# Kernel optimization log

Hardware: AMD Instinct MI355X
Metric: run time of the kernel (lower is better)

The kernel has to match this reference:

```python
import jax, jax.numpy as jnp
import numpy as np

RATIO = 0.1

def setup_inputs() -> dict:
    key = jax.random.key(0)
    x = jax.random.normal(key, (8, 1024, 4096), dtype=jnp.float32)
    return {"x": x}

def reference(x):
    shape = x.shape
    xf = x.reshape(-1)                       # [N]
    k = int(RATIO * xf.shape[0])             # static k
    src, index = jax.lax.top_k(xf, k)         # values (not abs), matching torch.topk
    out = jnp.zeros_like(xf).at[index].set(src)
    return out.reshape(shape)
```

## Files before the change

kernel.cpp:

```cpp
#include <hip/hip_runtime.h>
#include <stdint.h>


#define BLK       256
#define MAXGRID   1024
#define NB1       4096
#define NBC       1024
#define STAGE_CAP 3072
#define EQ_CAP    65536
#define GRP_SHIFT 6
#define LSTRIDE   64

typedef float vf4 __attribute__((ext_vector_type(4)));

__device__ __forceinline__ unsigned f2u(float x) {
    unsigned b = __float_as_uint(x);
    return (b & 0x80000000u) ? ~b : (b | 0x80000000u);
}
__device__ __forceinline__ float u2f(unsigned u) {
    return __uint_as_float((u & 0x80000000u) ? (u & 0x7FFFFFFFu) : ~u);
}
__device__ __forceinline__ unsigned cload(const unsigned* p) {
    return __hip_atomic_load(p, __ATOMIC_RELAXED, __HIP_MEMORY_SCOPE_AGENT);
}
__device__ __forceinline__ void cstore(unsigned* p, unsigned v) {
    __hip_atomic_store(p, v, __ATOMIC_RELAXED, __HIP_MEMORY_SCOPE_AGENT);
}

__device__ __forceinline__ void gsync(unsigned* bw, unsigned ep, unsigned nbk) {
    __syncthreads();
    if (threadIdx.x == 0) {
        const unsigned g  = (unsigned)blockIdx.x >> GRP_SHIFT;
        const unsigned ng = (nbk + ((1u << GRP_SHIFT) - 1u)) >> GRP_SHIFT;
        unsigned* arr = bw;
        unsigned* gar = bw + 1024;
        unsigned* rel = bw + 1088;
        unsigned grp0 = g << GRP_SHIFT;
        unsigned cnt_g = nbk - grp0;
        if (cnt_g > (1u << GRP_SHIFT)) cnt_g = (1u << GRP_SHIFT);
        unsigned old = __hip_atomic_fetch_add(&arr[g * LSTRIDE], 1u,
                                              __ATOMIC_RELAXED, __HIP_MEMORY_SCOPE_AGENT);
        if (old == ep * cnt_g - 1u) {
            unsigned og = __hip_atomic_fetch_add(gar, 1u,
                                                 __ATOMIC_RELAXED, __HIP_MEMORY_SCOPE_AGENT);
            if (og == ep * ng - 1u) {
                for (unsigned i = 0; i < ng; ++i)
                    cstore(&rel[i * LSTRIDE], ep);
            }
        }
        unsigned spins = 0u;
        while (cload(&rel[g * LSTRIDE]) < ep) {
            __builtin_amdgcn_s_sleep(16);
            if (++spins > 1500000u) break;
        }
    }
    __syncthreads();
}

__device__ __forceinline__ unsigned block_exscan256(unsigned v,
                                                    volatile unsigned* lds,
                                                    int tid)
{
    lds[tid] = v;
    __syncthreads();
    for (int off = 1; off < 256; off <<= 1) {
        unsigned t = (tid >= off) ? lds[tid - off] : 0u;
        __syncthreads();
        lds[tid] += t;
        __syncthreads();
    }
    unsigned incl = lds[tid];
    return incl - v;
}

template<int NB, int PT>
__device__ void scan_desc(const unsigned* h, unsigned kin,
                          volatile unsigned* slds, unsigned* sb, int tid)
{
    unsigned loc[PT], partial = 0u;
#pragma unroll
    for (int i = 0; i < PT; ++i) {
        loc[i] = cload(&h[NB - 1 - (tid * PT + i)]);
        partial += loc[i];
    }
    unsigned cum = block_exscan256(partial, slds, tid);
#pragma unroll
    for (int i = 0; i < PT; ++i) {
        unsigned c = loc[i];
        if (cum < kin && cum + c >= kin) {
            sb[0] = (unsigned)(NB - 1 - (tid * PT + i));
            sb[1] = kin - cum;
            sb[2] = c;
        }
        cum += c;
    }
    __syncthreads();
}

__global__ void __launch_bounds__(BLK, 4)
topk_fused(const float* __restrict__ x, float* __restrict__ out,
           long long N, int n4, unsigned k,
           unsigned* __restrict__ sc, unsigned* __restrict__ bw,
           unsigned* __restrict__ hist_a, unsigned* __restrict__ hist_b,
           unsigned* __restrict__ hist_c, unsigned* __restrict__ hist_b2,
           unsigned* __restrict__ hist_c2, unsigned* __restrict__ eq_list)
{
    __shared__ unsigned lh[2 * NB1];
    __shared__ unsigned slds[BLK];
    __shared__ unsigned sb[8];

    const int tid = threadIdx.x;
    const int bid = blockIdx.x;
    const unsigned nbk = gridDim.x;
    const int stride = (int)nbk * BLK;
    unsigned ep = 0;

    const float4* x4 = (const float4*)x;
    const long long t0 = (long long)n4 * 4;
    const int ntail = (int)(N - t0);

    for (int i = tid; i < 2 * NB1; i += BLK) lh[i] = 0u;
    __syncthreads();
    {
        unsigned* my = lh + ((tid >> 7) & 1) * NB1;
        for (int i = bid * BLK + tid; i < n4; i += stride) {
            float4 v = x4[i];
            atomicAdd(&my[f2u(v.x) >> 20], 1u);
            atomicAdd(&my[f2u(v.y) >> 20], 1u);
            atomicAdd(&my[f2u(v.z) >> 20], 1u);
            atomicAdd(&my[f2u(v.w) >> 20], 1u);
        }
        if (bid == 0 && tid < ntail) atomicAdd(&my[f2u(x[t0 + tid]) >> 20], 1u);
    }
    __syncthreads();
    for (int i = tid; i < NB1; i += BLK) {
        unsigned s = lh[i] + lh[NB1 + i];
        if (s) atomicAdd(&hist_a[i], s);
    }
    gsync(bw, ++ep, nbk);

    scan_desc<NB1, 16>(hist_a, k, slds, sb, tid);
    const unsigned b1 = sb[0], krem = sb[1];
    __syncthreads();

    if (tid == 0) sb[3] = 0u;
    __syncthreads();
    unsigned* su = lh;
    unsigned* si = lh + STAGE_CAP;
    auto stage = [&](unsigned u, unsigned idxv) {
        unsigned p = atomicAdd(&sb[3], 1u);
        if (p < STAGE_CAP) { su[p] = u; si[p] = idxv; }
        else cstore(&sc[7], 1u);
    };
    for (int i = bid * BLK + tid; i < n4; i += stride) {
        float4 v = x4[i];
        unsigned u0 = f2u(v.x), u1 = f2u(v.y), u2 = f2u(v.z), u3 = f2u(v.w);
        bool c0 = (u0 >> 20) == b1, c1 = (u1 >> 20) == b1,
             c2 = (u2 >> 20) == b1, c3 = (u3 >> 20) == b1;
        vf4 o;
        o.x = ((u0 >> 20) > b1) ? v.x : 0.0f;
        o.y = ((u1 >> 20) > b1) ? v.y : 0.0f;
        o.z = ((u2 >> 20) > b1) ? v.z : 0.0f;
        o.w = ((u3 >> 20) > b1) ? v.w : 0.0f;
        if (!(c0 | c1 | c2 | c3)) {
            __builtin_nontemporal_store(o, (vf4*)out + i);
        } else {
            unsigned base = (unsigned)i * 4u;
            if (c0) stage(u0, base + 0u); else out[base + 0u] = o.x;
            if (c1) stage(u1, base + 1u); else out[base + 1u] = o.y;
            if (c2) stage(u2, base + 2u); else out[base + 2u] = o.z;
            if (c3) stage(u3, base + 3u); else out[base + 3u] = o.w;
        }
    }
    if (bid == 0 && tid < ntail) {
        long long idx = t0 + tid;
        float v = x[idx];
        unsigned u = f2u(v);
        if ((u >> 20) == b1) stage(u, (unsigned)idx);
        else out[idx] = ((u >> 20) > b1) ? v : 0.0f;
    }
    __syncthreads();
    const unsigned mycnt0 = sb[3];
    const unsigned mycnt = (mycnt0 > STAGE_CAP) ? STAGE_CAP : mycnt0;
    unsigned* chist = lh + 2 * STAGE_CAP;
    unsigned* chm = chist + ((tid >> 7) & 1) * NBC;
    for (int i = tid; i < 2 * NBC; i += BLK) chist[i] = 0u;
    __syncthreads();
    for (unsigned j = (unsigned)tid; j < mycnt; j += BLK)
        atomicAdd(&chm[(su[j] >> 10) & 1023u], 1u);
    __syncthreads();
    for (int i = tid; i < NBC; i += BLK) {
        unsigned s = chist[i] + chist[NBC + i];
        if (s) atomicAdd(&hist_b[i], s);
    }
    gsync(bw, ++ep, nbk);

    const bool ovf = (cload(&sc[7]) != 0u);

    if (!ovf) {
        scan_desc<NBC, 4>(hist_b, krem, slds, sb, tid);
        const unsigned b2 = sb[0], krem2 = sb[1];
        __syncthreads();

        for (int i = tid; i < 2 * NBC; i += BLK) chist[i] = 0u;
        __syncthreads();
        for (unsigned j = (unsigned)tid; j < mycnt; j += BLK) {
            unsigned u = su[j];
            if (((u >> 10) & 1023u) == b2) atomicAdd(&chm[u & 1023u], 1u);
        }
        __syncthreads();
        for (int i = tid; i < NBC; i += BLK) {
            unsigned s = chist[i] + chist[NBC + i];
            if (s) atomicAdd(&hist_c[i], s);
        }
        gsync(bw, ++ep, nbk);

        scan_desc<NBC, 4>(hist_c, krem2, slds, sb, tid);
        const unsigned b3 = sb[0], needeq = sb[1], ceq = sb[2];
        const unsigned tu = (b1 << 20) | (b2 << 10) | b3;
        const bool allties = (needeq == ceq);

        for (unsigned j = (unsigned)tid; j < mycnt; j += BLK) {
            unsigned u = su[j], idxv = si[j];
            if (u > tu)      out[idxv] = u2f(u);
            else if (u < tu) out[idxv] = 0.0f;
            else if (allties) out[idxv] = u2f(u);
            else { unsigned q = atomicAdd(&sc[5], 1u); if (q < EQ_CAP) cstore(&eq_list[q], idxv); }
        }
        if (!allties) {
            gsync(bw, ++ep, nbk);
            if (bid == 0) {
                unsigned m = cload(&sc[5]); if (m > EQ_CAP) m = EQ_CAP;
                float f = u2f(tu);
                for (unsigned j = (unsigned)tid; j < m; j += BLK) {
                    unsigned idxv = cload(&eq_list[j]);
                    unsigned cnt = 0u;
                    for (unsigned l = 0; l < m; ++l)
                        cnt += (cload(&eq_list[l]) < idxv) ? 1u : 0u;
                    out[idxv] = (cnt < needeq) ? f : 0.0f;
                }
            }
        }
    } else {
        for (int i = tid; i < 2 * NBC; i += BLK) chist[i] = 0u;
        __syncthreads();
        for (int i = bid * BLK + tid; i < n4; i += stride) {
            float4 v = x4[i];
            unsigned u;
            u = f2u(v.x); if ((u >> 20) == b1) atomicAdd(&chm[(u >> 10) & 1023u], 1u);
            u = f2u(v.y); if ((u >> 20) == b1) atomicAdd(&chm[(u >> 10) & 1023u], 1u);
            u = f2u(v.z); if ((u >> 20) == b1) atomicAdd(&chm[(u >> 10) & 1023u], 1u);
            u = f2u(v.w); if ((u >> 20) == b1) atomicAdd(&chm[(u >> 10) & 1023u], 1u);
        }
        if (bid == 0 && tid < ntail) {
            unsigned u = f2u(x[t0 + tid]);
            if ((u >> 20) == b1) atomicAdd(&chm[(u >> 10) & 1023u], 1u);
        }
        __syncthreads();
        for (int i = tid; i < NBC; i += BLK) {
            unsigned s = chist[i] + chist[NBC + i];
            if (s) atomicAdd(&hist_b2[i], s);
        }
        gsync(bw, ++ep, nbk);
        scan_desc<NBC, 4>(hist_b2, krem, slds, sb, tid);
        const unsigned b2 = sb[0], krem2 = sb[1];
        __syncthreads();

        for (int i = tid; i < 2 * NBC; i += BLK) chist[i] = 0u;
        __syncthreads();
        for (int i = bid * BLK + tid; i < n4; i += stride) {
            float4 v = x4[i];
            unsigned u;
            u = f2u(v.x); if ((u >> 20) == b1 && ((u >> 10) & 1023u) == b2) atomicAdd(&chm[u & 1023u], 1u);
            u = f2u(v.y); if ((u >> 20) == b1 && ((u >> 10) & 1023u) == b2) atomicAdd(&chm[u & 1023u], 1u);
            u = f2u(v.z); if ((u >> 20) == b1 && ((u >> 10) & 1023u) == b2) atomicAdd(&chm[u & 1023u], 1u);
            u = f2u(v.w); if ((u >> 20) == b1 && ((u >> 10) & 1023u) == b2) atomicAdd(&chm[u & 1023u], 1u);
        }
        if (bid == 0 && tid < ntail) {
            unsigned u = f2u(x[t0 + tid]);
            if ((u >> 20) == b1 && ((u >> 10) & 1023u) == b2) atomicAdd(&chm[u & 1023u], 1u);
        }
        __syncthreads();
        for (int i = tid; i < NBC; i += BLK) {
            unsigned s = chist[i] + chist[NBC + i];
            if (s) atomicAdd(&hist_c2[i], s);
        }
        gsync(bw, ++ep, nbk);
        scan_desc<NBC, 4>(hist_c2, krem2, slds, sb, tid);
        const unsigned b3 = sb[0], needeq = sb[1], ceq = sb[2];
        const unsigned tu = (b1 << 20) | (b2 << 10) | b3;
        const bool allties = (needeq == ceq);

        for (int i = bid * BLK + tid; i < n4; i += stride) {
            float4 v = x4[i];
            unsigned base = (unsigned)i * 4u;
            unsigned uu[4] = { f2u(v.x), f2u(v.y), f2u(v.z), f2u(v.w) };
#pragma unroll
            for (int l = 0; l < 4; ++l) {
                unsigned u = uu[l];
                if ((u >> 20) == b1) {
                    if (u > tu)      out[base + l] = u2f(u);
                    else if (u < tu) out[base + l] = 0.0f;
                    else if (allties) out[base + l] = u2f(u);
                    else { unsigned q = atomicAdd(&sc[5], 1u); if (q < EQ_CAP) cstore(&eq_list[q], base + (unsigned)l); }
                }
            }
        }
        if (bid == 0 && tid < ntail) {
            long long idx = t0 + tid;
            unsigned u = f2u(x[idx]);
            if ((u >> 20) == b1) {
                if (u > tu)      out[idx] = u2f(u);
                else if (u < tu) out[idx] = 0.0f;
                else if (allties) out[idx] = u2f(u);
                else { unsigned q = atomicAdd(&sc[5], 1u); if (q < EQ_CAP) cstore(&eq_list[q], (unsigned)idx); }
            }
        }
        if (!allties) {
            gsync(bw, ++ep, nbk);
            if (bid == 0) {
                unsigned m = cload(&sc[5]); if (m > EQ_CAP) m = EQ_CAP;
                float f = u2f(tu);
                for (unsigned j = (unsigned)tid; j < m; j += BLK) {
                    unsigned idxv = cload(&eq_list[j]);
                    unsigned cnt = 0u;
                    for (unsigned l = 0; l < m; ++l)
                        cnt += (cload(&eq_list[l]) < idxv) ? 1u : 0u;
                    out[idxv] = (cnt < needeq) ? f : 0.0f;
                }
            }
        }
    }
}

extern "C" void kernel_launch(void* const* d_in, const int* in_sizes, int n_in,
                              void* d_out, int out_size, void* d_ws, size_t ws_size,
                              hipStream_t stream) {
    const float* x = (const float*)d_in[0];
    float* out = (float*)d_out;
    long long N = (long long)in_sizes[0];
    int n4 = (int)(N >> 2);
    unsigned k = (unsigned)((double)N * 0.1);
    if (k == 0u) k = 1u;

    uint8_t* w = (uint8_t*)d_ws;
    unsigned* sc      = (unsigned*)(w);
    unsigned* bw      = (unsigned*)(w + 256);
    unsigned* hist_a  = (unsigned*)(w + 256 + 12288);
    unsigned* hist_b  = hist_a + NB1;
    unsigned* hist_c  = hist_b + NBC;
    unsigned* hist_b2 = hist_c + NBC;
    unsigned* hist_c2 = hist_b2 + NBC;
    unsigned* eq_list = hist_c2 + NBC;
    const size_t zbytes = 256 + 12288 + (NB1 + 4 * NBC) * sizeof(unsigned);

    static int g_grid = 0;
    if (g_grid == 0) {
        int nb = 0;
        if (hipOccupancyMaxActiveBlocksPerMultiprocessor(&nb, (const void*)topk_fused,
                                                         BLK, 0) != hipSuccess || nb < 1)
            nb = 4;
        int dev = 0; (void)hipGetDevice(&dev);
        int ncu = 0;
        if (hipDeviceGetAttribute(&ncu, hipDeviceAttributeMultiprocessorCount, dev) != hipSuccess || ncu < 1)
            ncu = 256;
        long long g = (long long)nb * (long long)ncu;
        if (g > MAXGRID) g = MAXGRID;
        if (g < 1) g = 1;
        g_grid = (int)g;
    }

    (void)hipMemsetAsync(w, 0, zbytes, stream);
    hipLaunchKernelGGL(topk_fused, dim3(g_grid), dim3(BLK), 0, stream,
                       x, out, N, n4, k, sc, bw,
                       hist_a, hist_b, hist_c, hist_b2, hist_c2, eq_list);
}
```

Baseline: 335.8 us.

## Shrink LDS footprint to double occupancy and restructure radix digit split

Reduces the first-pass histogram to 2048 bins (11-bit digit) with a single LDS copy and shrinks the staging capacity, cutting shared memory so 8 blocks per CU fit and the persistent grid can grow to 2048 blocks. The second digit becomes 11 bits. The write pass now always issues a full vector nontemporal store and stages boundary-bucket elements separately. Tie resolution is spread across all blocks instead of block 0. Risks: more LDS atomic contention without privatized copies, more staging overflows into the slow fallback path, and costlier grid barriers with twice as many blocks.

```diff
diff --git a/kernel.cpp b/kernel.cpp
--- a/kernel.cpp
+++ b/kernel.cpp
@@ -3,10 +3,11 @@
 
 
 #define BLK       256
-#define MAXGRID   1024
-#define NB1       4096
-#define NBC       1024
-#define STAGE_CAP 3072
+#define MAXGRID   2048
+#define NB1       2048
+#define NC1       2048
+#define NC2       1024
+#define STAGE_CAP 1280
 #define EQ_CAP    65536
 #define GRP_SHIFT 6
 #define LSTRIDE   64
@@ -33,8 +34,8 @@
         const unsigned g  = (unsigned)blockIdx.x >> GRP_SHIFT;
         const unsigned ng = (nbk + ((1u << GRP_SHIFT) - 1u)) >> GRP_SHIFT;
         unsigned* arr = bw;
-        unsigned* gar = bw + 1024;
-        unsigned* rel = bw + 1088;
+        unsigned* gar = bw + 2048;
+        unsigned* rel = bw + 2112;
         unsigned grp0 = g << GRP_SHIFT;
         unsigned cnt_g = nbk - grp0;
         if (cnt_g > (1u << GRP_SHIFT)) cnt_g = (1u << GRP_SHIFT);
@@ -50,8 +51,8 @@
         }
         unsigned spins = 0u;
         while (cload(&rel[g * LSTRIDE]) < ep) {
-            __builtin_amdgcn_s_sleep(16);
-            if (++spins > 1500000u) break;
+            __builtin_amdgcn_s_sleep(8);
+            if (++spins > 3000000u) break;
         }
     }
     __syncthreads();
@@ -97,7 +98,7 @@
     __syncthreads();
 }
 
-__global__ void __launch_bounds__(BLK, 4)
+__global__ void __launch_bounds__(BLK, 8)
 topk_fused(const float* __restrict__ x, float* __restrict__ out,
            long long N, int n4, unsigned k,
            unsigned* __restrict__ sc, unsigned* __restrict__ bw,
@@ -105,7 +106,7 @@
            unsigned* __restrict__ hist_c, unsigned* __restrict__ hist_b2,
            unsigned* __restrict__ hist_c2, unsigned* __restrict__ eq_list)
 {
-    __shared__ unsigned lh[2 * NB1];
+    __shared__ unsigned lh[2 * STAGE_CAP + NC1];
     __shared__ unsigned slds[BLK];
     __shared__ unsigned sb[8];
 
@@ -119,27 +120,24 @@
     const long long t0 = (long long)n4 * 4;
     const int ntail = (int)(N - t0);
 
-    for (int i = tid; i < 2 * NB1; i += BLK) lh[i] = 0u;
-    __syncthreads();
-    {
-        unsigned* my = lh + ((tid >> 7) & 1) * NB1;
-        for (int i = bid * BLK + tid; i < n4; i += stride) {
-            float4 v = x4[i];
-            atomicAdd(&my[f2u(v.x) >> 20], 1u);
-            atomicAdd(&my[f2u(v.y) >> 20], 1u);
-            atomicAdd(&my[f2u(v.z) >> 20], 1u);
-            atomicAdd(&my[f2u(v.w) >> 20], 1u);
-        }
-        if (bid == 0 && tid < ntail) atomicAdd(&my[f2u(x[t0 + tid]) >> 20], 1u);
-    }
+    for (int i = tid; i < NB1; i += BLK) lh[i] = 0u;
+    __syncthreads();
+    for (int i = bid * BLK + tid; i < n4; i += stride) {
+        float4 v = x4[i];
+        atomicAdd(&lh[f2u(v.x) >> 21], 1u);
+        atomicAdd(&lh[f2u(v.y) >> 21], 1u);
+        atomicAdd(&lh[f2u(v.z) >> 21], 1u);
+        atomicAdd(&lh[f2u(v.w) >> 21], 1u);
+    }
+    if (bid == 0 && tid < ntail) atomicAdd(&lh[f2u(x[t0 + tid]) >> 21], 1u);
     __syncthreads();
     for (int i = tid; i < NB1; i += BLK) {
-        unsigned s = lh[i] + lh[NB1 + i];
+        unsigned s = lh[i];
         if (s) atomicAdd(&hist_a[i], s);
     }
     gsync(bw, ++ep, nbk);
 
-    scan_desc<NB1, 16>(hist_a, k, slds, sb, tid);
+    scan_desc<NB1, NB1 / BLK>(hist_a, k, slds, sb, tid);
     const unsigned b1 = sb[0], krem = sb[1];
     __syncthreads();
 
@@ -147,6 +145,7 @@
     __syncthreads();
     unsigned* su = lh;
     unsigned* si = lh + STAGE_CAP;
+    unsigned* chist = lh + 2 * STAGE_CAP;
     auto stage = [&](unsigned u, unsigned idxv) {
         unsigned p = atomicAdd(&sb[3], 1u);
         if (p < STAGE_CAP) { su[p] = u; si[p] = idxv; }
@@ -155,42 +154,38 @@
     for (int i = bid * BLK + tid; i < n4; i += stride) {
         float4 v = x4[i];
         unsigned u0 = f2u(v.x), u1 = f2u(v.y), u2 = f2u(v.z), u3 = f2u(v.w);
-        bool c0 = (u0 >> 20) == b1, c1 = (u1 >> 20) == b1,
-             c2 = (u2 >> 20) == b1, c3 = (u3 >> 20) == b1;
         vf4 o;
-        o.x = ((u0 >> 20) > b1) ? v.x : 0.0f;
-        o.y = ((u1 >> 20) > b1) ? v.y : 0.0f;
-        o.z = ((u2 >> 20) > b1) ? v.z : 0.0f;
-        o.w = ((u3 >> 20) > b1) ? v.w : 0.0f;
-        if (!(c0 | c1 | c2 | c3)) {
-            __builtin_nontemporal_store(o, (vf4*)out + i);
-        } else {
+        o.x = ((u0 >> 21) > b1) ? v.x : 0.0f;
+        o.y = ((u1 >> 21) > b1) ? v.y : 0.0f;
+        o.z = ((u2 >> 21) > b1) ? v.z : 0.0f;
+        o.w = ((u3 >> 21) > b1) ? v.w : 0.0f;
+        __builtin_nontemporal_store(o, (vf4*)out + i);
+        if (((u0 >> 21) == b1) | ((u1 >> 21) == b1) |
+            ((u2 >> 21) == b1) | ((u3 >> 21) == b1)) {
             unsigned base = (unsigned)i * 4u;
-            if (c0) stage(u0, base + 0u); else out[base + 0u] = o.x;
-            if (c1) stage(u1, base + 1u); else out[base + 1u] = o.y;
-            if (c2) stage(u2, base + 2u); else out[base + 2u] = o.z;
-            if (c3) stage(u3, base + 3u); else out[base + 3u] = o.w;
+            if ((u0 >> 21) == b1) stage(u0, base + 0u);
+            if ((u1 >> 21) == b1) stage(u1, base + 1u);
+            if ((u2 >> 21) == b1) stage(u2, base + 2u);
+            if ((u3 >> 21) == b1) stage(u3, base + 3u);
         }
     }
     if (bid == 0 && tid < ntail) {
         long long idx = t0 + tid;
         float v = x[idx];
         unsigned u = f2u(v);
-        if ((u >> 20) == b1) stage(u, (unsigned)idx);
-        else out[idx] = ((u >> 20) > b1) ? v : 0.0f;
+        out[idx] = ((u >> 21) > b1) ? v : 0.0f;
+        if ((u >> 21) == b1) stage(u, (unsigned)idx);
     }
     __syncthreads();
     const unsigned mycnt0 = sb[3];
     const unsigned mycnt = (mycnt0 > STAGE_CAP) ? STAGE_CAP : mycnt0;
-    unsigned* chist = lh + 2 * STAGE_CAP;
-    unsigned* chm = chist + ((tid >> 7) & 1) * NBC;
-    for (int i = tid; i < 2 * NBC; i += BLK) chist[i] = 0u;
+    for (int i = tid; i < NC1; i += BLK) chist[i] = 0u;
     __syncthreads();
     for (unsigned j = (unsigned)tid; j < mycnt; j += BLK)
-        atomicAdd(&chm[(su[j] >> 10) & 1023u], 1u);
-    __syncthreads();
-    for (int i = tid; i < NBC; i += BLK) {
-        unsigned s = chist[i] + chist[NBC + i];
+        atomicAdd(&chist[(su[j] >> 10) & (NC1 - 1u)], 1u);
+    __syncthreads();
+    for (int i = tid; i < NC1; i += BLK) {
+        unsigned s = chist[i];
         if (s) atomicAdd(&hist_b[i], s);
     }
     gsync(bw, ++ep, nbk);
@@ -198,97 +193,99 @@
     const bool ovf = (cload(&sc[7]) != 0u);
 
     if (!ovf) {
-        scan_desc<NBC, 4>(hist_b, krem, slds, sb, tid);
+        scan_desc<NC1, NC1 / BLK>(hist_b, krem, slds, sb, tid);
         const unsigned b2 = sb[0], krem2 = sb[1];
         __syncthreads();
 
-        for (int i = tid; i < 2 * NBC; i += BLK) chist[i] = 0u;
+        for (int i = tid; i < NC2; i += BLK) chist[i] = 0u;
         __syncthreads();
         for (unsigned j = (unsigned)tid; j < mycnt; j += BLK) {
             unsigned u = su[j];
-            if (((u >> 10) & 1023u) == b2) atomicAdd(&chm[u & 1023u], 1u);
-        }
-        __syncthreads();
-        for (int i = tid; i < NBC; i += BLK) {
-            unsigned s = chist[i] + chist[NBC + i];
+            if (((u >> 10) & (NC1 - 1u)) == b2) atomicAdd(&chist[u & (NC2 - 1u)], 1u);
+        }
+        __syncthreads();
+        for (int i = tid; i < NC2; i += BLK) {
+            unsigned s = chist[i];
             if (s) atomicAdd(&hist_c[i], s);
         }
         gsync(bw, ++ep, nbk);
 
-        scan_desc<NBC, 4>(hist_c, krem2, slds, sb, tid);
+        scan_desc<NC2, NC2 / BLK>(hist_c, krem2, slds, sb, tid);
         const unsigned b3 = sb[0], needeq = sb[1], ceq = sb[2];
-        const unsigned tu = (b1 << 20) | (b2 << 10) | b3;
+        const unsigned tu = (b1 << 21) | (b2 << 10) | b3;
         const bool allties = (needeq == ceq);
 
         for (unsigned j = (unsigned)tid; j < mycnt; j += BLK) {
-            unsigned u = su[j], idxv = si[j];
-            if (u > tu)      out[idxv] = u2f(u);
-            else if (u < tu) out[idxv] = 0.0f;
-            else if (allties) out[idxv] = u2f(u);
-            else { unsigned q = atomicAdd(&sc[5], 1u); if (q < EQ_CAP) cstore(&eq_list[q], idxv); }
+            unsigned u = su[j];
+            if (u > tu)                  out[si[j]] = u2f(u);
+            else if (u == tu) {
+                if (allties)             out[si[j]] = u2f(u);
+                else { unsigned q = atomicAdd(&sc[5], 1u);
+                       if (q < EQ_CAP) cstore(&eq_list[q], si[j]); }
+            }
         }
         if (!allties) {
             gsync(bw, ++ep, nbk);
-            if (bid == 0) {
-                unsigned m = cload(&sc[5]); if (m > EQ_CAP) m = EQ_CAP;
-                float f = u2f(tu);
-                for (unsigned j = (unsigned)tid; j < m; j += BLK) {
-                    unsigned idxv = cload(&eq_list[j]);
-                    unsigned cnt = 0u;
-                    for (unsigned l = 0; l < m; ++l)
-                        cnt += (cload(&eq_list[l]) < idxv) ? 1u : 0u;
-                    out[idxv] = (cnt < needeq) ? f : 0.0f;
-                }
+            unsigned m = cload(&sc[5]); if (m > EQ_CAP) m = EQ_CAP;
+            float f = u2f(tu);
+            for (unsigned j = (unsigned)tid; j < mycnt; j += BLK) {
+                unsigned u = su[j];
+                if (u != tu) continue;
+                unsigned idxv = si[j];
+                unsigned cnt = 0u;
+                for (unsigned l = 0; l < m; ++l)
+                    cnt += (cload(&eq_list[l]) < idxv) ? 1u : 0u;
+                if (cnt < needeq) out[idxv] = f;
             }
         }
     } else {
-        for (int i = tid; i < 2 * NBC; i += BLK) chist[i] = 0u;
+        for (int i = tid; i < NC1; i += BLK) chist[i] = 0u;
         __syncthreads();
         for (int i = bid * BLK + tid; i < n4; i += stride) {
             float4 v = x4[i];
             unsigned u;
-            u = f2u(v.x); if ((u >> 20) == b1) atomicAdd(&chm[(u >> 10) & 1023u], 1u);
-            u = f2u(v.y); if ((u >> 20) == b1) atomicAdd(&chm[(u >> 10) & 1023u], 1u);
-            u = f2u(v.z); if ((u >> 20) == b1) atomicAdd(&chm[(u >> 10) & 1023u], 1u);
-            u = f2u(v.w); if ((u >> 20) == b1) atomicAdd(&chm[(u >> 10) & 1023u], 1u);
+            u = f2u(v.x); if ((u >> 21) == b1) atomicAdd(&chist[(u >> 10) & (NC1 - 1u)], 1u);
+            u = f2u(v.y); if ((u >> 21) == b1) atomicAdd(&chist[(u >> 10) & (NC1 - 1u)], 1u);
+            u = f2u(v.z); if ((u >> 21) == b1) atomicAdd(&chist[(u >> 10) & (NC1 - 1u)], 1u);
+            u = f2u(v.w); if ((u >> 21) == b1) atomicAdd(&chist[(u >> 10) & (NC1 - 1u)], 1u);
         }
         if (bid == 0 && tid < ntail) {
             unsigned u = f2u(x[t0 + tid]);
-            if ((u >> 20) == b1) atomicAdd(&chm[(u >> 10) & 1023u], 1u);
-        }
-        __syncthreads();
-        for (int i = tid; i < NBC; i += BLK) {
-            unsigned s = chist[i] + chist[NBC + i];
+            if ((u >> 21) == b1) atomicAdd(&chist[(u >> 10) & (NC1 - 1u)], 1u);
+        }
+        __syncthreads();
+        for (int i = tid; i < NC1; i += BLK) {
+            unsigned s = chist[i];
             if (s) atomicAdd(&hist_b2[i], s);
         }
         gsync(bw, ++ep, nbk);
-        scan_desc<NBC, 4>(hist_b2, krem, slds, sb, tid);
+        scan_desc<NC1, NC1 / BLK>(hist_b2, krem, slds, sb, tid);
         const unsigned b2 = sb[0], krem2 = sb[1];
         __syncthreads();
 
-        for (int i = tid; i < 2 * NBC; i += BLK) chist[i] = 0u;
+        for (int i = tid; i < NC2; i += BLK) chist[i] = 0u;
         __syncthreads();
         for (int i = bid * BLK + tid; i < n4; i += stride) {
             float4 v = x4[i];
             unsigned u;
-            u = f2u(v.x); if ((u >> 20) == b1 && ((u >> 10) & 1023u) == b2) atomicAdd(&chm[u & 1023u], 1u);
-            u = f2u(v.y); if ((u >> 20) == b1 && ((u >> 10) & 1023u) == b2) atomicAdd(&chm[u & 1023u], 1u);
-            u = f2u(v.z); if ((u >> 20) == b1 && ((u >> 10) & 1023u) == b2) atomicAdd(&chm[u & 1023u], 1u);
-            u = f2u(v.w); if ((u >> 20) == b1 && ((u >> 10) & 1023u) == b2) atomicAdd(&chm[u & 1023u], 1u);
+            u = f2u(v.x); if ((u >> 21) == b1 && ((u >> 10) & (NC1 - 1u)) == b2) atomicAdd(&chist[u & (NC2 - 1u)], 1u);
+            u = f2u(v.y); if ((u >> 21) == b1 && ((u >> 10) & (NC1 - 1u)) == b2) atomicAdd(&chist[u & (NC2 - 1u)], 1u);
+            u = f2u(v.z); if ((u >> 21) == b1 && ((u >> 10) & (NC1 - 1u)) == b2) atomicAdd(&chist[u & (NC2 - 1u)], 1u);
+            u = f2u(v.w); if ((u >> 21) == b1 && ((u >> 10) & (NC1 - 1u)) == b2) atomicAdd(&chist[u & (NC2 - 1u)], 1u);
         }
         if (bid == 0 && tid < ntail) {
             unsigned u = f2u(x[t0 + tid]);
-            if ((u >> 20) == b1 && ((u >> 10) & 1023u) == b2) atomicAdd(&chm[u & 1023u], 1u);
-        }
-        __syncthreads();
-        for (int i = tid; i < NBC; i += BLK) {
-            unsigned s = chist[i] + chist[NBC + i];
+            if ((u >> 21) == b1 && ((u >> 10) & (NC1 - 1u)) == b2) atomicAdd(&chist[u & (NC2 - 1u)], 1u);
+        }
+        __syncthreads();
+        for (int i = tid; i < NC2; i += BLK) {
+            unsigned s = chist[i];
             if (s) atomicAdd(&hist_c2[i], s);
         }
         gsync(bw, ++ep, nbk);
-        scan_desc<NBC, 4>(hist_c2, krem2, slds, sb, tid);
+        scan_desc<NC2, NC2 / BLK>(hist_c2, krem2, slds, sb, tid);
         const unsigned b3 = sb[0], needeq = sb[1], ceq = sb[2];
-        const unsigned tu = (b1 << 20) | (b2 << 10) | b3;
+        const unsigned tu = (b1 << 21) | (b2 << 10) | b3;
         const bool allties = (needeq == ceq);
 
         for (int i = bid * BLK + tid; i < n4; i += stride) {
@@ -298,35 +295,52 @@
 #pragma unroll
             for (int l = 0; l < 4; ++l) {
                 unsigned u = uu[l];
-                if ((u >> 20) == b1) {
-                    if (u > tu)      out[base + l] = u2f(u);
-                    else if (u < tu) out[base + l] = 0.0f;
-                    else if (allties) out[base + l] = u2f(u);
-                    else { unsigned q = atomicAdd(&sc[5], 1u); if (q < EQ_CAP) cstore(&eq_list[q], base + (unsigned)l); }
+                if ((u >> 21) != b1) continue;
+                if (u > tu)                  out[base + l] = u2f(u);
+                else if (u == tu) {
+                    if (allties)             out[base + l] = u2f(u);
+                    else { unsigned q = atomicAdd(&sc[5], 1u);
+                           if (q < EQ_CAP) cstore(&eq_list[q], base + (unsigned)l); }
                 }
             }
         }
         if (bid == 0 && tid < ntail) {
             long long idx = t0 + tid;
             unsigned u = f2u(x[idx]);
-            if ((u >> 20) == b1) {
-                if (u > tu)      out[idx] = u2f(u);
-                else if (u < tu) out[idx] = 0.0f;
-                else if (allties) out[idx] = u2f(u);
-                else { unsigned q = atomicAdd(&sc[5], 1u); if (q < EQ_CAP) cstore(&eq_list[q], (unsigned)idx); }
+            if ((u >> 21) == b1) {
+                if (u > tu)                  out[idx] = u2f(u);
+                else if (u == tu) {
+                    if (allties)             out[idx] = u2f(u);
+                    else { unsigned q = atomicAdd(&sc[5], 1u);
+                           if (q < EQ_CAP) cstore(&eq_list[q], (unsigned)idx); }
+                }
             }
         }
         if (!allties) {
             gsync(bw, ++ep, nbk);
-            if (bid == 0) {
-                unsigned m = cload(&sc[5]); if (m > EQ_CAP) m = EQ_CAP;
-                float f = u2f(tu);
-                for (unsigned j = (unsigned)tid; j < m; j += BLK) {
-                    unsigned idxv = cload(&eq_list[j]);
+            unsigned m = cload(&sc[5]); if (m > EQ_CAP) m = EQ_CAP;
+            float f = u2f(tu);
+            for (int i = bid * BLK + tid; i < n4; i += stride) {
+                float4 v = x4[i];
+                unsigned base = (unsigned)i * 4u;
+                unsigned uu[4] = { f2u(v.x), f2u(v.y), f2u(v.z), f2u(v.w) };
+#pragma unroll
+                for (int l = 0; l < 4; ++l) {
+                    if (uu[l] != tu) continue;
+                    unsigned idxv = base + (unsigned)l;
                     unsigned cnt = 0u;
-                    for (unsigned l = 0; l < m; ++l)
-                        cnt += (cload(&eq_list[l]) < idxv) ? 1u : 0u;
-                    out[idxv] = (cnt < needeq) ? f : 0.0f;
+                    for (unsigned q = 0; q < m; ++q)
+                        cnt += (cload(&eq_list[q]) < idxv) ? 1u : 0u;
+                    if (cnt < needeq) out[idxv] = f;
+                }
+            }
+            if (bid == 0 && tid < ntail) {
+                long long idx = t0 + tid;
+                if (f2u(x[idx]) == tu) {
+                    unsigned cnt = 0u;
+                    for (unsigned q = 0; q < m; ++q)
+                        cnt += (cload(&eq_list[q]) < (unsigned)idx) ? 1u : 0u;
+                    if (cnt < needeq) out[idx] = f;
                 }
             }
         }
@@ -346,20 +360,21 @@
     uint8_t* w = (uint8_t*)d_ws;
     unsigned* sc      = (unsigned*)(w);
     unsigned* bw      = (unsigned*)(w + 256);
-    unsigned* hist_a  = (unsigned*)(w + 256 + 12288);
+    unsigned* hist_a  = (unsigned*)(w + 256 + 20480);
     unsigned* hist_b  = hist_a + NB1;
-    unsigned* hist_c  = hist_b + NBC;
-    unsigned* hist_b2 = hist_c + NBC;
-    unsigned* hist_c2 = hist_b2 + NBC;
-    unsigned* eq_list = hist_c2 + NBC;
-    const size_t zbytes = 256 + 12288 + (NB1 + 4 * NBC) * sizeof(unsigned);
+    unsigned* hist_c  = hist_b + NC1;
+    unsigned* hist_b2 = hist_c + NC2;
+    unsigned* hist_c2 = hist_b2 + NC1;
+    unsigned* eq_list = hist_c2 + NC2;
+    const size_t zbytes = 256 + 20480 +
+        (size_t)(NB1 + NC1 + NC2 + NC1 + NC2) * sizeof(unsigned);
 
     static int g_grid = 0;
     if (g_grid == 0) {
         int nb = 0;
         if (hipOccupancyMaxActiveBlocksPerMultiprocessor(&nb, (const void*)topk_fused,
                                                          BLK, 0) != hipSuccess || nb < 1)
-            nb = 4;
+            nb = 8;
         int dev = 0; (void)hipGetDevice(&dev);
         int ncu = 0;
         if (hipDeviceGetAttribute(&ncu, hipDeviceAttributeMultiprocessorCount, dev) != hipSuccess || ncu < 1)
```

New measurement: 535.2 us. +59.4%, slower.
